# Kernel optimization log

Measured on AMD Instinct MI355X. Metric: run time of the kernel, lower is better.

The kernel has to match this reference:

```python
import jax, jax.numpy as jnp
import numpy as np
from jax import lax

STRIDE = 2
PAD = 2
K = 5

def conv_transpose3d(x, w, b):
    # x: (N, Cin, D, H, W); w: (Cin, Cout, kD, kH, kW) torch layout
    # Equivalent dense conv: flip kernel spatially, swap in/out, lhs-dilate by stride,
    # pad each side by (K - 1 - PAD).
    w_t = jnp.flip(w, axis=(2, 3, 4)).transpose(1, 0, 2, 3, 4)  # (Cout, Cin, kD, kH, kW)
    p = K - 1 - PAD  # = 2
    y = lax.conv_general_dilated(
        x, w_t,
        window_strides=(1, 1, 1),
        padding=[(p, p)] * 3,
        lhs_dilation=(STRIDE,) * 3,
        dimension_numbers=('NCDHW', 'OIDHW', 'NCDHW'))
    return y + b[None, :, None, None, None]

def maxpool3d(x, k):
    return lax.reduce_window(
        x, -jnp.inf, lax.max,
        window_dimensions=(1, 1, k, k, k),
        window_strides=(1, 1, k, k, k),
        padding='VALID')

def setup_inputs() -> dict:
    key = jax.random.key(0)
    k1, k2, k3 = jax.random.split(key, 3)
    x = jax.random.normal(k1, (16, 32, 16, 32, 32), dtype=jnp.float32)
    weight = jax.random.normal(k2, (32, 64, 5, 5, 5), dtype=jnp.float32) * 0.05
    bias = jax.random.normal(k3, (64,), dtype=jnp.float32) * 0.05
    return {"x": x, "weight": weight, "bias": bias}

def reference(x, weight, bias):
    y = conv_transpose3d(x, weight, bias)      # (16, 64, 31, 63, 63)
    y = maxpool3d(y, 2)                        # (16, 64, 15, 31, 31)
    y = maxpool3d(y, 3)                        # (16, 64, 5, 10, 10)
    return jnp.sum(y, axis=1, keepdims=True)   # (16, 1, 5, 10, 10)
```

## Files before the change

kernel.cpp:

```cpp
#include <hip/hip_runtime.h>

typedef short v8s __attribute__((ext_vector_type(8)));
typedef float v4f __attribute__((ext_vector_type(4)));

#define N_  16
#define CI_ 32
#define CO_ 64
#define DI  16
#define HI  32
#define WI  32
#define NEGINF (-__builtin_inff())

__device__ __forceinline__ unsigned short f2bf(float f) {
    unsigned int u = __float_as_uint(f);
    unsigned int r = (u + 0x7FFFu + ((u >> 16) & 1u)) >> 16;
    return (unsigned short)r;
}

__device__ __forceinline__ void gld16(const void* g, void* l) {
    __builtin_amdgcn_global_load_lds(
        (const __attribute__((address_space(1))) void*)g,
        (__attribute__((address_space(3))) void*)l, 16, 0, 0);
}

__constant__ int O64c[9] = {0, 55296, 92160, 129024, 153600, 190464, 215040, 239616, 256000};

__global__ void prep(const float* __restrict__ x, const float* __restrict__ w,
                     unsigned short* __restrict__ xp, unsigned short* __restrict__ wt,
                     int do_x) {
    if (blockIdx.x < 1088) {
        if (!do_x) return;
        __shared__ __align__(16) unsigned short tl[8192];
        const int bi = blockIdx.x;
        const int pd = bi % 17;
        const int cg = (bi / 17) & 3;
        const int n  = bi / 68;
        if (pd > 0) {
            const int c = threadIdx.x >> 5;
            const int ww = threadIdx.x & 31;
            const float* xc = x + (((size_t)(n * 32 + cg * 8 + c) * 16 + (pd - 1)) * 32) * 32;
            #pragma unroll
            for (int h = 0; h < 32; ++h)
                tl[(h * 32 + ww) * 8 + c] = f2bf(xc[h * 32 + ww]);
        }
        __syncthreads();
        unsigned short* xpo = xp + (size_t)bi * 8448;
        for (int o = threadIdx.x; o < 1056; o += 256) {
            int ph = o / 33, pw = o - ph * 33;
            v8s v;
            if (pd == 0 || ph == 0 || pw == 0) v = (v8s){0, 0, 0, 0, 0, 0, 0, 0};
            else v = *(const v8s*)&tl[((ph - 1) * 32 + pw - 1) * 8];
            *(v8s*)(xpo + o * 8) = v;
        }
    } else {
        int u = (blockIdx.x - 1088) * 256 + threadIdx.x;
        if (u >= 256000) return;
        int r = 0;
        #pragma unroll
        for (int i = 1; i < 8; ++i) r += (u >= O64c[i]);
        const int rd = r >> 2, rh = (r >> 1) & 1, rw = r & 1;
        const int nh = rh ? 2 : 3, nw = rw ? 2 : 3;
        int t2 = u - O64c[r];
        int j   = t2 & 7;
        int l   = (t2 >> 3) & 15;
        int q   = (t2 >> 7) & 3;
        int nt  = (t2 >> 9) & 3;
        int tap = t2 >> 11;
        int co = nt * 16 + l;
        int ci = q * 8 + j;
        int jw = tap % nw;
        int jh = (tap / nw) % nh;
        int jd = tap / (nw * nh);
        int kd = rd + 2 * jd, kh = rh + 2 * jh, kw = rw + 2 * jw;
        wt[u] = f2bf(w[(ci * CO_ + co) * 125 + kd * 25 + kh * 5 + kw]);
    }
}

__device__ __forceinline__ void run_class_rt(
        const unsigned short* __restrict__ xs,
        int laneAB,
        const unsigned short* __restrict__ wcls,
        const int taps, const int nw, const int nh, const bool par,
        unsigned Bm, bool isQ3, float (&pmax)[4][2])
{
    const int R0 = par ? 288 : 0;
    const int R1 = par ? 1440 : 576;
    const int R2 = par ? 2016 : 1728;
    const int R3_ = par ? 3168 : 2880;

    const char* xb = (const char*)xs;

    v4f acc[5][4];
    #pragma unroll
    for (int t = 0; t < 5; ++t)
        #pragma unroll
        for (int nt = 0; nt < 4; ++nt)
            acc[t][nt] = (v4f){0.f, 0.f, 0.f, 0.f};

    v8s B0[4], B1[4];
    #pragma unroll
    for (int nt = 0; nt < 4; ++nt) B0[nt] = *(const v8s*)(wcls + nt * 512);

    int aoff = 0, jw = 0, jh = 0;
    auto adv = [&]() {
        aoff += 16; ++jw;
        if (jw == nw) { jw = 0; aoff += 288 - 16 * nw; ++jh;
            if (jh == nh) { jh = 0; aoff += 1440 - 288 * nh; } }
    };
    auto comp = [&](const v8s (&B)[4]) {
        const int va = laneAB - aoff;
        v8s a0 = *(const v8s*)(xb + va + R0);
        v8s a1 = *(const v8s*)(xb + va + R1);
        v8s a2 = *(const v8s*)(xb + va + R2);
        v8s a3 = *(const v8s*)(xb + va + R3_);
        #pragma unroll
        for (int nt = 0; nt < 4; ++nt) {
            acc[0][nt] = __builtin_amdgcn_mfma_f32_16x16x32_bf16(a0, B[nt], acc[0][nt], 0, 0, 0);
            acc[1][nt] = __builtin_amdgcn_mfma_f32_16x16x32_bf16(a1, B[nt], acc[1][nt], 0, 0, 0);
            acc[2][nt] = __builtin_amdgcn_mfma_f32_16x16x32_bf16(a2, B[nt], acc[2][nt], 0, 0, 0);
            acc[3][nt] = __builtin_amdgcn_mfma_f32_16x16x32_bf16(a3, B[nt], acc[3][nt], 0, 0, 0);
        }
        if (!par) {
            v8s a4 = *(const v8s*)(xb + va + 3456);
            #pragma unroll
            for (int nt = 0; nt < 4; ++nt)
                acc[4][nt] = __builtin_amdgcn_mfma_f32_16x16x32_bf16(a4, B[nt], acc[4][nt], 0, 0, 0);
        }
    };

    int s = 0;
    while (s + 2 <= taps) {
        #pragma unroll
        for (int nt = 0; nt < 4; ++nt)
            B1[nt] = *(const v8s*)(wcls + ((s + 1) * 4 + nt) * 512);
        comp(B0); adv();
        if (s + 2 < taps) {
            #pragma unroll
            for (int nt = 0; nt < 4; ++nt)
                B0[nt] = *(const v8s*)(wcls + ((s + 2) * 4 + nt) * 512);
        }
        comp(B1); adv();
        s += 2;
    }
    if (s < taps) comp(B0);

    #pragma unroll
    for (int nt = 0; nt < 4; ++nt) {
        #pragma unroll
        for (int reg = 0; reg < 4; ++reg) {
            float v = acc[0][nt][reg];
            v = fmaxf(v, acc[1][nt][reg]);
            v = fmaxf(v, acc[2][nt][reg]);
            v = fmaxf(v, acc[3][nt][reg]);
            if (!par) v = fmaxf(v, acc[4][nt][reg]);
            if (reg == 3) v = isQ3 ? NEGINF : v;
            const bool bB = (Bm >> reg) & 1u;
            pmax[nt][0] = fmaxf(pmax[nt][0], bB ? NEGINF : v);
            pmax[nt][1] = fmaxf(pmax[nt][1], bB ? v : NEGINF);
        }
    }
}

template<bool PRE>
__global__ __launch_bounds__(256, 3)
void fused_main(const float* __restrict__ x, const unsigned short* __restrict__ xp,
                const unsigned short* __restrict__ wt,
                const float* __restrict__ bias, float* __restrict__ out) {
    __shared__ __align__(16) char smem[28800];
    unsigned short* xs = (unsigned short*)smem;
    float* P = (float*)smem;
    float* Y = (float*)(smem + 9472);

    const int b = blockIdx.x;
    const int whalf = b & 1;
    const int hj = (b >> 1) % 10;
    const int dj = (b / 20) % 5;
    const int n  = b / 100;

    const int lane = threadIdx.x & 63;
    const int wv   = threadIdx.x >> 6;

    if (PRE) {
        const int t = threadIdx.x;
        #pragma unroll
        for (int i = 0; i < 8; ++i) {
            int c = i * 256 + t;
            if (c < 1800) {
                int row = c / 18;
                int iwc = c - row * 18;
                int cg  = row / 25;
                int rr  = row - cg * 25;
                int idl = rr / 5;
                int ihl = rr - idl * 5;
                size_t goff = ((((size_t)((n * 4 + cg) * 17 + 3 * dj + idl)) * 32
                                + 3 * hj + ihl) * 33 + 15 * whalf + iwc) * 8;
                gld16(xp + goff, smem + i * 4096 + wv * 1024);
            }
        }
    } else {
        const int id0 = 3 * dj - 1, ih0 = 3 * hj - 1, iwb = 15 * whalf - 1;
        const float* xn = x + (size_t)n * (CI_ * DI * HI * WI);
        for (int e = threadIdx.x; e < 14400; e += 256) {
            int ci   = e / 450;
            int rem  = e - ci * 450;
            int idp  = rem / 90;
            int rem2 = rem - idp * 90;
            int ihp  = rem2 / 18;
            int iwp  = rem2 - ihp * 18;
            int id = id0 + idp, ih = ih0 + ihp, iw = iwb + iwp;
            float v = 0.f;
            if (id >= 0 && ih >= 0 && iw >= 0)
                v = xn[((ci * DI + id) * HI + ih) * WI + iw];
            xs[(ci >> 3) * 3600 + idp * 720 + ihp * 144 + iwp * 8 + (ci & 7)] = f2bf(v);
        }
    }
    __syncthreads();

    const int l = lane & 15, q = lane >> 4;
    const int laneAB = q * 7200 + (l + 2) * 16 + 3456;

    static constexpr int PT[4][2] = {{0, 7}, {1, 3}, {2, 5}, {4, 6}};
    static constexpr int tapsT[8] = {27, 18, 18, 12, 18, 12, 12, 8};
    static constexpr int O64[8]   = {0, 55296, 92160, 129024, 153600, 190464, 215040, 239616};
    static constexpr int nwT[8]   = {3, 2, 3, 2, 3, 2, 3, 2};
    static constexpr int nhT[8]   = {3, 3, 2, 2, 3, 3, 2, 2};

    float pmax[4][2];
    #pragma unroll
    for (int nt = 0; nt < 4; ++nt) { pmax[nt][0] = NEGINF; pmax[nt][1] = NEGINF; }

    const unsigned Bm = (0x0EC8u >> (q << 2)) & 0xFu;
    const bool isQ3 = (q == 3);

    #pragma unroll 1
    for (int it = 0; it < 4; ++it) {
        const bool par = (it & 1) != 0;
        const int  r   = PT[wv][it >> 1];
        run_class_rt(xs, laneAB, wt + O64[r] + lane * 8,
                     tapsT[r], nwT[r], nhT[r], par, Bm, isQ3, pmax);
    }

    __syncthreads();
    {
        int base = ((wv * 4 + q) * 16 + l) * 9;
        #pragma unroll
        for (int nt = 0; nt < 4; ++nt) {
            P[base + nt * 2 + 0] = pmax[nt][0];
            P[base + nt * 2 + 1] = pmax[nt][1];
        }
    }
    __syncthreads();

    static constexpr int wjAt[4] = {0, 1, 2, 4};
    static constexpr int wjBt[4] = {1, 2, 3, 5};
    for (int oi = threadIdx.x; oi < 320; oi += 256) {
        int co = oi / 5;
        int wjl = oi - co * 5;
        int lc = co & 15, ntc = co >> 4;
        float v = NEGINF;
        #pragma unroll
        for (int w = 0; w < 4; ++w) {
            #pragma unroll
            for (int qq = 0; qq < 4; ++qq) {
                const float* pp = &P[((w * 4 + qq) * 16 + lc) * 9 + ntc * 2];
                if (wjAt[qq] == wjl) v = fmaxf(v, pp[0]);
                if (wjBt[qq] == wjl) v = fmaxf(v, pp[1]);
            }
        }
        Y[co * 5 + wjl] = v + bias[co];
    }
    __syncthreads();

    if (wv == 0) {
        float vy[5];
        #pragma unroll
        for (int wjl = 0; wjl < 5; ++wjl) vy[wjl] = Y[lane * 5 + wjl];
        #pragma unroll
        for (int wjl = 0; wjl < 5; ++wjl) {
            float v = vy[wjl];
            #pragma unroll
            for (int off = 32; off > 0; off >>= 1)
                v += __shfl_down(v, off, 64);
            if (lane == 0)
                out[((n * 5 + dj) * 10 + hj) * 10 + whalf * 5 + wjl] = v;
        }
    }
}

extern "C" void kernel_launch(void* const* d_in, const int* in_sizes, int n_in,
                              void* d_out, int out_size, void* d_ws, size_t ws_size,
                              hipStream_t stream) {
    const float* x    = (const float*)d_in[0];
    const float* w    = (const float*)d_in[1];
    const float* bias = (const float*)d_in[2];
    float*       out  = (float*)d_out;
    unsigned short* wt = (unsigned short*)d_ws;
    unsigned short* xp = (unsigned short*)((char*)d_ws + 512512);
    const size_t XP_NEED = 512512 + 18382848;
    const int do_x = (ws_size >= XP_NEED) ? 1 : 0;

    prep<<<dim3(2088), 256, 0, stream>>>(x, w, xp, wt, do_x);
    if (do_x)
        fused_main<true ><<<dim3(1600), 256, 0, stream>>>(x, xp, wt, bias, out);
    else
        fused_main<false><<<dim3(1600), 256, 0, stream>>>(x, xp, wt, bias, out);
}
```

Measured before the change: 193.1 us.

## Split tail tiles across output-channel groups and rebalance per-wave work units

The last 64 tiles, which form a partial wave of blocks, are each split into four blocks, one per 16-channel group, and the partial sums are combined with atomicAdd into an output that prep zeroes. The per-wave work assignment is also rebalanced: each wave now runs a variable list of (class, parity) units instead of a fixed two-class pair. The aim is to shrink the tail-wave imbalance across CUs and even out the MFMA work per wave. In exchange the tail tiles redundantly reload the input tile four times, and the result now depends on atomics and on prep running first.

```diff
diff --git a/kernel.cpp b/kernel.cpp
--- a/kernel.cpp
+++ b/kernel.cpp
@@ -27,7 +27,7 @@
 
 __global__ void prep(const float* __restrict__ x, const float* __restrict__ w,
                      unsigned short* __restrict__ xp, unsigned short* __restrict__ wt,
-                     int do_x) {
+                     float* __restrict__ out, int do_x) {
     if (blockIdx.x < 1088) {
         if (!do_x) return;
         __shared__ __align__(16) unsigned short tl[8192];
@@ -53,6 +53,13 @@
             *(v8s*)(xpo + o * 8) = v;
         }
     } else {
+        if (blockIdx.x == 1088 && threadIdx.x < 64) {
+            int tb = 1536 + threadIdx.x;
+            int whalf = tb & 1, hj = (tb >> 1) % 10, dj = (tb / 20) % 5, n = tb / 100;
+            float* o = out + (((size_t)(n * 5 + dj) * 10 + hj) * 10 + whalf * 5);
+            #pragma unroll
+            for (int j = 0; j < 5; ++j) o[j] = 0.f;
+        }
         int u = (blockIdx.x - 1088) * 256 + threadIdx.x;
         if (u >= 256000) return;
         int r = 0;
@@ -161,6 +168,73 @@
     }
 }
 
+__device__ __forceinline__ void run_class_nt1(
+        const unsigned short* __restrict__ xs,
+        int laneAB,
+        const unsigned short* __restrict__ wcls,
+        const int taps, const int nw, const int nh, const bool par,
+        unsigned Bm, bool isQ3, float (&pmax)[2])
+{
+    const int R0 = par ? 288 : 0;
+    const int R1 = par ? 1440 : 576;
+    const int R2 = par ? 2016 : 1728;
+    const int R3_ = par ? 3168 : 2880;
+
+    const char* xb = (const char*)xs;
+
+    v4f acc[5];
+    #pragma unroll
+    for (int t = 0; t < 5; ++t) acc[t] = (v4f){0.f, 0.f, 0.f, 0.f};
+
+    v8s B0 = *(const v8s*)(wcls);
+    v8s B1;
+
+    int aoff = 0, jw = 0, jh = 0;
+    auto adv = [&]() {
+        aoff += 16; ++jw;
+        if (jw == nw) { jw = 0; aoff += 288 - 16 * nw; ++jh;
+            if (jh == nh) { jh = 0; aoff += 1440 - 288 * nh; } }
+    };
+    auto comp = [&](v8s B) {
+        const int va = laneAB - aoff;
+        v8s a0 = *(const v8s*)(xb + va + R0);
+        v8s a1 = *(const v8s*)(xb + va + R1);
+        v8s a2 = *(const v8s*)(xb + va + R2);
+        v8s a3 = *(const v8s*)(xb + va + R3_);
+        acc[0] = __builtin_amdgcn_mfma_f32_16x16x32_bf16(a0, B, acc[0], 0, 0, 0);
+        acc[1] = __builtin_amdgcn_mfma_f32_16x16x32_bf16(a1, B, acc[1], 0, 0, 0);
+        acc[2] = __builtin_amdgcn_mfma_f32_16x16x32_bf16(a2, B, acc[2], 0, 0, 0);
+        acc[3] = __builtin_amdgcn_mfma_f32_16x16x32_bf16(a3, B, acc[3], 0, 0, 0);
+        if (!par) {
+            v8s a4 = *(const v8s*)(xb + va + 3456);
+            acc[4] = __builtin_amdgcn_mfma_f32_16x16x32_bf16(a4, B, acc[4], 0, 0, 0);
+        }
+    };
+
+    int s = 0;
+    while (s + 2 <= taps) {
+        B1 = *(const v8s*)(wcls + (s + 1) * 2048);
+        comp(B0); adv();
+        if (s + 2 < taps) B0 = *(const v8s*)(wcls + (s + 2) * 2048);
+        comp(B1); adv();
+        s += 2;
+    }
+    if (s < taps) comp(B0);
+
+    #pragma unroll
+    for (int reg = 0; reg < 4; ++reg) {
+        float v = acc[0][reg];
+        v = fmaxf(v, acc[1][reg]);
+        v = fmaxf(v, acc[2][reg]);
+        v = fmaxf(v, acc[3][reg]);
+        if (!par) v = fmaxf(v, acc[4][reg]);
+        if (reg == 3) v = isQ3 ? NEGINF : v;
+        const bool bB = (Bm >> reg) & 1u;
+        pmax[0] = fmaxf(pmax[0], bB ? NEGINF : v);
+        pmax[1] = fmaxf(pmax[1], bB ? v : NEGINF);
+    }
+}
+
 template<bool PRE>
 __global__ __launch_bounds__(256, 3)
 void fused_main(const float* __restrict__ x, const unsigned short* __restrict__ xp,
@@ -172,10 +246,15 @@
     float* Y = (float*)(smem + 9472);
 
     const int b = blockIdx.x;
-    const int whalf = b & 1;
-    const int hj = (b >> 1) % 10;
-    const int dj = (b / 20) % 5;
-    const int n  = b / 100;
+    const bool tail = (b >= 1536);
+    int tile, sub;
+    if (tail) { int u = b - 1536; tile = 1536 + (u >> 2); sub = u & 3; }
+    else      { tile = b; sub = 0; }
+
+    const int whalf = tile & 1;
+    const int hj = (tile >> 1) % 10;
+    const int dj = (tile / 20) % 5;
+    const int n  = tile / 100;
 
     const int lane = threadIdx.x & 63;
     const int wv   = threadIdx.x >> 6;
@@ -219,70 +298,126 @@
     const int l = lane & 15, q = lane >> 4;
     const int laneAB = q * 7200 + (l + 2) * 16 + 3456;
 
-    static constexpr int PT[4][2] = {{0, 7}, {1, 3}, {2, 5}, {4, 6}};
     static constexpr int tapsT[8] = {27, 18, 18, 12, 18, 12, 12, 8};
     static constexpr int O64[8]   = {0, 55296, 92160, 129024, 153600, 190464, 215040, 239616};
     static constexpr int nwT[8]   = {3, 2, 3, 2, 3, 2, 3, 2};
     static constexpr int nhT[8]   = {3, 3, 2, 2, 3, 3, 2, 2};
-
-    float pmax[4][2];
-    #pragma unroll
-    for (int nt = 0; nt < 4; ++nt) { pmax[nt][0] = NEGINF; pmax[nt][1] = NEGINF; }
+    static constexpr int uOff[5] = {0, 3, 7, 11, 16};
+    static constexpr int uR[16] = {0,0,7,  1,2,4,7,  4,1,2,3,  3,5,6,5,6};
+    static constexpr int uP[16] = {0,1,0,  0,0,1,1,  0,1,1,1,  0,0,0,1,1};
+
+    static constexpr int wjAt[4] = {0, 1, 2, 4};
+    static constexpr int wjBt[4] = {1, 2, 3, 5};
 
     const unsigned Bm = (0x0EC8u >> (q << 2)) & 0xFu;
     const bool isQ3 = (q == 3);
-
-    #pragma unroll 1
-    for (int it = 0; it < 4; ++it) {
-        const bool par = (it & 1) != 0;
-        const int  r   = PT[wv][it >> 1];
-        run_class_rt(xs, laneAB, wt + O64[r] + lane * 8,
-                     tapsT[r], nwT[r], nhT[r], par, Bm, isQ3, pmax);
-    }
-
-    __syncthreads();
-    {
-        int base = ((wv * 4 + q) * 16 + l) * 9;
-        #pragma unroll
-        for (int nt = 0; nt < 4; ++nt) {
-            P[base + nt * 2 + 0] = pmax[nt][0];
-            P[base + nt * 2 + 1] = pmax[nt][1];
-        }
-    }
-    __syncthreads();
-
-    static constexpr int wjAt[4] = {0, 1, 2, 4};
-    static constexpr int wjBt[4] = {1, 2, 3, 5};
-    for (int oi = threadIdx.x; oi < 320; oi += 256) {
-        int co = oi / 5;
-        int wjl = oi - co * 5;
-        int lc = co & 15, ntc = co >> 4;
-        float v = NEGINF;
-        #pragma unroll
-        for (int w = 0; w < 4; ++w) {
-            #pragma unroll
-            for (int qq = 0; qq < 4; ++qq) {
-                const float* pp = &P[((w * 4 + qq) * 16 + lc) * 9 + ntc * 2];
-                if (wjAt[qq] == wjl) v = fmaxf(v, pp[0]);
-                if (wjBt[qq] == wjl) v = fmaxf(v, pp[1]);
-            }
-        }
-        Y[co * 5 + wjl] = v + bias[co];
-    }
-    __syncthreads();
-
-    if (wv == 0) {
-        float vy[5];
-        #pragma unroll
-        for (int wjl = 0; wjl < 5; ++wjl) vy[wjl] = Y[lane * 5 + wjl];
-        #pragma unroll
-        for (int wjl = 0; wjl < 5; ++wjl) {
-            float v = vy[wjl];
-            #pragma unroll
-            for (int off = 32; off > 0; off >>= 1)
-                v += __shfl_down(v, off, 64);
-            if (lane == 0)
-                out[((n * 5 + dj) * 10 + hj) * 10 + whalf * 5 + wjl] = v;
+    const int u0 = uOff[wv], u1 = uOff[wv + 1];
+
+    if (!tail) {
+        float pmax[4][2];
+        #pragma unroll
+        for (int nt = 0; nt < 4; ++nt) { pmax[nt][0] = NEGINF; pmax[nt][1] = NEGINF; }
+
+        #pragma unroll 1
+        for (int iu = u0; iu < u1; ++iu) {
+            const int  r   = uR[iu];
+            const bool par = uP[iu] != 0;
+            run_class_rt(xs, laneAB, wt + O64[r] + lane * 8,
+                         tapsT[r], nwT[r], nhT[r], par, Bm, isQ3, pmax);
+        }
+
+        __syncthreads();
+        {
+            int base = ((wv * 4 + q) * 16 + l) * 9;
+            #pragma unroll
+            for (int nt = 0; nt < 4; ++nt) {
+                P[base + nt * 2 + 0] = pmax[nt][0];
+                P[base + nt * 2 + 1] = pmax[nt][1];
+            }
+        }
+        __syncthreads();
+
+        for (int oi = threadIdx.x; oi < 320; oi += 256) {
+            int co = oi / 5;
+            int wjl = oi - co * 5;
+            int lc = co & 15, ntc = co >> 4;
+            float v = NEGINF;
+            #pragma unroll
+            for (int w = 0; w < 4; ++w) {
+                #pragma unroll
+                for (int qq = 0; qq < 4; ++qq) {
+                    const float* pp = &P[((w * 4 + qq) * 16 + lc) * 9 + ntc * 2];
+                    if (wjAt[qq] == wjl) v = fmaxf(v, pp[0]);
+                    if (wjBt[qq] == wjl) v = fmaxf(v, pp[1]);
+                }
+            }
+            Y[co * 5 + wjl] = v + bias[co];
+        }
+        __syncthreads();
+
+        if (wv == 0) {
+            float vy[5];
+            #pragma unroll
+            for (int wjl = 0; wjl < 5; ++wjl) vy[wjl] = Y[lane * 5 + wjl];
+            #pragma unroll
+            for (int wjl = 0; wjl < 5; ++wjl) {
+                float v = vy[wjl];
+                #pragma unroll
+                for (int off = 32; off > 0; off >>= 1)
+                    v += __shfl_down(v, off, 64);
+                if (lane == 0)
+                    out[((n * 5 + dj) * 10 + hj) * 10 + whalf * 5 + wjl] = v;
+            }
+        }
+    } else {
+        float pmax1[2];
+        pmax1[0] = NEGINF; pmax1[1] = NEGINF;
+
+        #pragma unroll 1
+        for (int iu = u0; iu < u1; ++iu) {
+            const int  r   = uR[iu];
+            const bool par = uP[iu] != 0;
+            run_class_nt1(xs, laneAB, wt + O64[r] + sub * 512 + lane * 8,
+                          tapsT[r], nwT[r], nhT[r], par, Bm, isQ3, pmax1);
+        }
+
+        __syncthreads();
+        {
+            int base = ((wv * 4 + q) * 16 + l) * 9;
+            P[base + sub * 2 + 0] = pmax1[0];
+            P[base + sub * 2 + 1] = pmax1[1];
+        }
+        __syncthreads();
+
+        if (wv == 0) {
+            const int co = lane;
+            const int lc = co & 15, ntc = co >> 4;
+            const bool valid = (ntc == sub);
+            float vy[5];
+            #pragma unroll
+            for (int wjl = 0; wjl < 5; ++wjl) vy[wjl] = NEGINF;
+            #pragma unroll
+            for (int w = 0; w < 4; ++w) {
+                #pragma unroll
+                for (int qq = 0; qq < 4; ++qq) {
+                    const float* pp = &P[((w * 4 + qq) * 16 + lc) * 9 + sub * 2];
+                    float a = pp[0], bv = pp[1];
+                    #pragma unroll
+                    for (int wjl = 0; wjl < 5; ++wjl) {
+                        if (wjAt[qq] == wjl) vy[wjl] = fmaxf(vy[wjl], a);
+                        if (wjBt[qq] == wjl) vy[wjl] = fmaxf(vy[wjl], bv);
+                    }
+                }
+            }
+            #pragma unroll
+            for (int wjl = 0; wjl < 5; ++wjl) {
+                float v = valid ? (vy[wjl] + bias[co]) : 0.f;
+                #pragma unroll
+                for (int off = 32; off > 0; off >>= 1)
+                    v += __shfl_down(v, off, 64);
+                if (lane == 0)
+                    atomicAdd(&out[((n * 5 + dj) * 10 + hj) * 10 + whalf * 5 + wjl], v);
+            }
         }
     }
 }
@@ -299,9 +434,9 @@
     const size_t XP_NEED = 512512 + 18382848;
     const int do_x = (ws_size >= XP_NEED) ? 1 : 0;
 
-    prep<<<dim3(2088), 256, 0, stream>>>(x, w, xp, wt, do_x);
+    prep<<<dim3(2088), 256, 0, stream>>>(x, w, xp, wt, out, do_x);
     if (do_x)
-        fused_main<true ><<<dim3(1600), 256, 0, stream>>>(x, xp, wt, bias, out);
+        fused_main<true ><<<dim3(1792), 256, 0, stream>>>(x, xp, wt, bias, out);
     else
-        fused_main<false><<<dim3(1600), 256, 0, stream>>>(x, xp, wt, bias, out);
-}
+        fused_main<false><<<dim3(1792), 256, 0, stream>>>(x, xp, wt, bias, out);
+}
```

After: 183.1 us. 1.05x faster.
